# Optimization experiments

Hardware: AMD Instinct MI355X
Metric: run time of the kernel (lower is better)

Reference implementation:

```python
import jax, jax.numpy as jnp
import numpy as np

T, B, IN, H, OUT = 345, 128, 13, 128, 9

# snnTorch ATan surrogate spike: forward = heaviside(x), backward = 1/(1+(pi*x)^2) (alpha=2)
@jax.custom_vjp
def spike_fn(x):
    return (x > 0).astype(x.dtype)

def _spike_fwd(x):
    return spike_fn(x), x

def _spike_bwd(x, g):
    return (g / (1.0 + (jnp.pi * x) ** 2),)

spike_fn.defvjp(_spike_fwd, _spike_bwd)


def setup_inputs() -> dict:
    key = jax.random.key(0)
    ks = jax.random.split(key, 5)
    x = jax.random.normal(ks[0], (B, IN, T), dtype=jnp.float32)
    # PyTorch Linear init: U(-1/sqrt(fan_in), 1/sqrt(fan_in))
    lim1 = 1.0 / np.sqrt(IN)
    lim2 = 1.0 / np.sqrt(H)
    W1 = jax.random.uniform(ks[1], (H, IN), minval=-lim1, maxval=lim1, dtype=jnp.float32)
    b1 = jax.random.uniform(ks[2], (H,), minval=-lim1, maxval=lim1, dtype=jnp.float32)
    W2 = jax.random.uniform(ks[3], (OUT, H), minval=-lim2, maxval=lim2, dtype=jnp.float32)
    b2 = jax.random.uniform(ks[4], (OUT,), minval=-lim2, maxval=lim2, dtype=jnp.float32)
    beta1 = jnp.float32(0.9)
    thr1 = jnp.float32(1.0)
    beta2 = jnp.float32(0.9)
    thr2 = jnp.float32(1.0)
    return {"x": x, "W1": W1, "b1": b1, "W2": W2, "b2": b2,
            "beta1": beta1, "thr1": thr1, "beta2": beta2, "thr2": thr2}


def reference(x, W1, b1, W2, b2, beta1, thr1, beta2, thr2):
    # Precompute fc1 for all steps: (T, B, H)
    cur1_all = jnp.einsum('bct,hc->tbh', x, W1) + b1
    bt1 = jnp.clip(beta1, 0.0, 1.0)
    bt2 = jnp.clip(beta2, 0.0, 1.0)

    def step(carry, cur1):
        mem1, mem2 = carry
        mem1 = bt1 * mem1 + cur1                 # leaky integrate
        spk1 = spike_fn(mem1 - thr1)             # fire
        mem1 = mem1 - spk1 * thr1                # subtract reset
        cur2 = spk1 @ W2.T + b2                  # (B, OUT)
        mem2 = bt2 * mem2 + cur2
        spk2 = spike_fn(mem2 - thr2)
        mem2 = mem2 - spk2 * thr2
        return (mem1, mem2), (spk2, mem2)

    init = (jnp.zeros((B, H), x.dtype), jnp.zeros((B, OUT), x.dtype))
    _, (spk_rec, mem_rec) = jax.lax.scan(step, init, cur1_all)
    return spk_rec, mem_rec  # each (T, B, OUT)
```

## Files before the change

### kernel.cpp

```cpp
#include <hip/hip_runtime.h>

#define T_STEPS 345
#define B_SZ    128
#define IN_SZ   13
#define H_SZ    128
#define OUT_SZ  9
#define XPITCH  16
#define TPAD    384
#define CPAD    388
#define NBO     (B_SZ * OUT_SZ)

__global__ __launch_bounds__(512, 2)
void snn_fused(const float* __restrict__ x, const float* __restrict__ W1,
               const float* __restrict__ b1, const float* __restrict__ W2,
               const float* __restrict__ b2,
               const float* __restrict__ beta1p, const float* __restrict__ thr1p,
               const float* __restrict__ beta2p, const float* __restrict__ thr2p,
               float* __restrict__ out)
{
    const int b    = blockIdx.x >> 1;
    const int half = blockIdx.x & 1;
    const int tid  = threadIdx.x;

    __shared__ float xst[(T_STEPS + 3) * XPITCH];
    __shared__ unsigned long long msh[TPAD * 2];
    __shared__ float c2s[OUT_SZ * CPAD];

    const float* xb = x + (size_t)b * (IN_SZ * T_STEPS);
    for (int i = tid; i < IN_SZ * T_STEPS; i += 512) {
        const int c = i / T_STEPS;
        const int t = i - c * T_STEPS;
        xst[t * XPITCH + c] = xb[i];
    }
    __syncthreads();

    if (tid < 128) {
        const float bt1 = fminf(fmaxf(beta1p[0], 0.0f), 1.0f);
        const float th1 = thr1p[0];

        float w1r[IN_SZ];
#pragma unroll
        for (int c = 0; c < IN_SZ; ++c) w1r[c] = W1[tid * IN_SZ + c];
        const float b1r = b1[tid];

        float mem1 = 0.0f;
        unsigned long long* mp = msh + (tid >> 6);
        const bool store_lane = (tid & 63) == 0;

        const float4* xq = (const float4*)xst;
        float4 a0 = xq[0], a1 = xq[1], a2 = xq[2]; float a3 = xst[12];
        float4 c0 = xq[4], c1 = xq[5], c2 = xq[6]; float c3 = xst[XPITCH + 12];

        int t = 0;
        for (; t < T_STEPS - 1; t += 2) {
            const float xa[IN_SZ] = { a0.x,a0.y,a0.z,a0.w, a1.x,a1.y,a1.z,a1.w,
                                      a2.x,a2.y,a2.z,a2.w, a3 };
            const float xc[IN_SZ] = { c0.x,c0.y,c0.z,c0.w, c1.x,c1.y,c1.z,c1.w,
                                      c2.x,c2.y,c2.z,c2.w, c3 };
            a0 = xq[(t+2)*4+0]; a1 = xq[(t+2)*4+1]; a2 = xq[(t+2)*4+2]; a3 = xst[(t+2)*XPITCH+12];
            c0 = xq[(t+3)*4+0]; c1 = xq[(t+3)*4+1]; c2 = xq[(t+3)*4+2]; c3 = xst[(t+3)*XPITCH+12];

            float cura = b1r, curb = b1r;
#pragma unroll
            for (int c = 0; c < IN_SZ; ++c) {
                cura = fmaf(xa[c], w1r[c], cura);
                curb = fmaf(xc[c], w1r[c], curb);
            }

            mem1 = fmaf(bt1, mem1, cura);
            const bool pa = mem1 > th1;
            const unsigned long long ma = __ballot(pa);
            mem1 = fmaf(pa ? -1.0f : 0.0f, th1, mem1);
            if (store_lane) mp[0] = ma;

            mem1 = fmaf(bt1, mem1, curb);
            const bool pb = mem1 > th1;
            const unsigned long long mb = __ballot(pb);
            mem1 = fmaf(pb ? -1.0f : 0.0f, th1, mem1);
            if (store_lane) mp[2] = mb;

            mp += 4;
        }
        {
            const float xa[IN_SZ] = { a0.x,a0.y,a0.z,a0.w, a1.x,a1.y,a1.z,a1.w,
                                      a2.x,a2.y,a2.z,a2.w, a3 };
            float cura = b1r;
#pragma unroll
            for (int c = 0; c < IN_SZ; ++c) cura = fmaf(xa[c], w1r[c], cura);
            mem1 = fmaf(bt1, mem1, cura);
            const bool pa = mem1 > th1;
            const unsigned long long ma = __ballot(pa);
            if (store_lane) mp[0] = ma;
        }
    }
    __syncthreads();

    {
        const int wave = tid >> 6;
        const int lane = tid & 63;
        const int tstart = half ? 30 : 0;
        const int tend   = half ? 54 : 30;
        for (int task = tstart + wave; task < tend; task += 8) {
            const int o  = task / 6;
            const int w  = task - o * 6;
            const int t  = w * 64 + lane;
            const int tc = (t < T_STEPS) ? t : (T_STEPS - 1);

            const uint4 mm = *(const uint4*)((const char*)msh + (size_t)tc * 16);

            const float* __restrict__ w2row = W2 + o * H_SZ;
            float acc = 0.0f;
#pragma unroll
            for (int h = 0; h < 32; ++h)
                acc = fmaf((float)((mm.x >> h) & 1u), w2row[h], acc);
#pragma unroll
            for (int h = 0; h < 32; ++h)
                acc = fmaf((float)((mm.y >> h) & 1u), w2row[32 + h], acc);
#pragma unroll
            for (int h = 0; h < 32; ++h)
                acc = fmaf((float)((mm.z >> h) & 1u), w2row[64 + h], acc);
#pragma unroll
            for (int h = 0; h < 32; ++h)
                acc = fmaf((float)((mm.w >> h) & 1u), w2row[96 + h], acc);

            c2s[o * CPAD + t] = acc + b2[o];
        }
    }
    __syncthreads();

    {
        const int nrows = half ? 4 : 5;
        if (tid < nrows) {
            const int o = (half ? 5 : 0) + tid;
            const float bt2 = fminf(fmaxf(beta2p[0], 0.0f), 1.0f);
            const float th2 = thr2p[0];
            const int lid = b * OUT_SZ + o;

            const float4* __restrict__ src = (const float4*)(c2s + o * CPAD);
            float* __restrict__ out_spk = out + lid;
            float* __restrict__ out_mem = out + (size_t)T_STEPS * NBO + lid;

            float mem2 = 0.0f;
            float4 f0 = src[0], f1 = src[1], f2 = src[2], f3 = src[3];

            for (int g = 0; g < 88; g += 4) {
                const float4 u0 = f0, u1 = f1, u2 = f2, u3 = f3;
                f0 = src[g + 4]; f1 = src[g + 5]; f2 = src[g + 6]; f3 = src[g + 7];

                const float4 us[4] = { u0, u1, u2, u3 };
#pragma unroll
                for (int j = 0; j < 4; ++j) {
                    const float vv[4] = { us[j].x, us[j].y, us[j].z, us[j].w };
#pragma unroll
                    for (int k = 0; k < 4; ++k) {
                        const int tt = (g + j) * 4 + k;
                        mem2 = fmaf(bt2, mem2, vv[k]);
                        const float s2 = (mem2 > th2) ? 1.0f : 0.0f;
                        mem2 = fmaf(-s2, th2, mem2);
                        if (tt < T_STEPS) {
                            out_spk[(size_t)tt * NBO] = s2;
                            out_mem[(size_t)tt * NBO] = mem2;
                        }
                    }
                }
            }
        }
    }
}

extern "C" void kernel_launch(void* const* d_in, const int* in_sizes, int n_in,
                              void* d_out, int out_size, void* d_ws, size_t ws_size,
                              hipStream_t stream) {
    const float* x     = (const float*)d_in[0];
    const float* W1    = (const float*)d_in[1];
    const float* b1    = (const float*)d_in[2];
    const float* W2    = (const float*)d_in[3];
    const float* b2    = (const float*)d_in[4];
    const float* beta1 = (const float*)d_in[5];
    const float* thr1  = (const float*)d_in[6];
    const float* beta2 = (const float*)d_in[7];
    const float* thr2  = (const float*)d_in[8];
    float* out = (float*)d_out;
    (void)in_sizes; (void)n_in; (void)out_size; (void)d_ws; (void)ws_size;

    snn_fused<<<dim3(B_SZ * 2), dim3(512), 0, stream>>>(
        x, W1, b1, W2, b2, beta1, thr1, beta2, thr2, out);
}
```

Baseline: 123.9 us.

## Pipeline fc1 precompute and layer-2 scan alongside the serial recurrences

Moves the fc1 matmul off the serial mem1 scan. Waves 2-7 compute cur1 for the next 92-step chunk into a double-buffered shared array while waves 0-1 scan the current chunk. The W2 projection is then split into 64-step slices, and wave 7 runs the layer-2 scan on slice s-1 while the other waves compute slice s. The aim is to shorten the serial critical path. In exchange it uses much more shared memory (about 100 KB for the cur1 buffers), which may lower occupancy, and it adds a block barrier per stage.

```diff
diff --git a/kernel.cpp b/kernel.cpp
--- a/kernel.cpp
+++ b/kernel.cpp
@@ -5,10 +5,76 @@
 #define IN_SZ   13
 #define H_SZ    128
 #define OUT_SZ  9
-#define XPITCH  16
-#define TPAD    384
 #define CPAD    388
 #define NBO     (B_SZ * OUT_SZ)
+#define CHUNK   92
+#define BUFR    100
+
+
+__device__ __forceinline__ void emit_cur1(float* __restrict__ buf,
+                                          const float* __restrict__ xst,
+                                          const float (&w1r)[4][IN_SZ],
+                                          const float (&b1r)[4],
+                                          int T0, int L, int hq, int off, int stride)
+{
+    for (int tl = off; tl < L; tl += stride) {
+        const int t = T0 + tl;
+        const float4* xq = (const float4*)(xst + t * 16);
+        const float4 x0 = xq[0], x1 = xq[1], x2 = xq[2];
+        const float x12 = xst[t * 16 + 12];
+        const float xa[IN_SZ] = { x0.x,x0.y,x0.z,x0.w, x1.x,x1.y,x1.z,x1.w,
+                                  x2.x,x2.y,x2.z,x2.w, x12 };
+        float* brow = buf + tl * H_SZ + hq;
+#pragma unroll
+        for (int k2 = 0; k2 < 4; ++k2) {
+            float cur = b1r[k2];
+#pragma unroll
+            for (int c = 0; c < IN_SZ; ++c) cur = fmaf(xa[c], w1r[k2][c], cur);
+            brow[k2 * 32] = cur;
+        }
+    }
+}
+
+__device__ __forceinline__ void scan1_step(float& mem1, float u, float bt1, float th1,
+                                           unsigned long long* __restrict__ msh,
+                                           int t, bool sl, int half)
+{
+    mem1 = fmaf(bt1, mem1, u);
+    const bool p = mem1 > th1;
+    const unsigned long long m = __ballot(p);
+    const float ms = mem1 - th1;
+    mem1 = p ? ms : mem1;
+    if (sl) msh[t * 2 + half] = m;
+}
+
+__device__ __forceinline__ void scan1_chunk(const float* __restrict__ buf,
+                                            unsigned long long* __restrict__ msh,
+                                            int T0, int L, int h,
+                                            float bt1, float th1, float& mem1)
+{
+    const float* cb = buf + h;
+    const bool sl = (h & 63) == 0;
+    const int half = h >> 6;
+    float a0 = cb[0*128], a1 = cb[1*128], a2 = cb[2*128], a3 = cb[3*128];
+    float b0 = cb[4*128], b1v = cb[5*128], b2v = cb[6*128], b3 = cb[7*128];
+    const int fullg = L >> 2;
+    const int rem   = L & 3;
+    for (int g = 0; g < fullg; ++g) {
+        const float u0 = a0, u1 = a1, u2 = a2, u3 = a3;
+        a0 = b0; a1 = b1v; a2 = b2v; a3 = b3;
+        const float* nb = cb + (g + 2) * 4 * 128;
+        b0 = nb[0]; b1v = nb[128]; b2v = nb[256]; b3 = nb[384];
+        const int tb = T0 + g * 4;
+        scan1_step(mem1, u0, bt1, th1, msh, tb + 0, sl, half);
+        scan1_step(mem1, u1, bt1, th1, msh, tb + 1, sl, half);
+        scan1_step(mem1, u2, bt1, th1, msh, tb + 2, sl, half);
+        scan1_step(mem1, u3, bt1, th1, msh, tb + 3, sl, half);
+    }
+    const int tb = T0 + fullg * 4;
+    if (rem > 0) scan1_step(mem1, a0, bt1, th1, msh, tb + 0, sl, half);
+    if (rem > 1) scan1_step(mem1, a1, bt1, th1, msh, tb + 1, sl, half);
+    if (rem > 2) scan1_step(mem1, a2, bt1, th1, msh, tb + 2, sl, half);
+}
 
 __global__ __launch_bounds__(512, 2)
 void snn_fused(const float* __restrict__ x, const float* __restrict__ W1,
@@ -21,147 +87,131 @@
     const int b    = blockIdx.x >> 1;
     const int half = blockIdx.x & 1;
     const int tid  = threadIdx.x;
-
-    __shared__ float xst[(T_STEPS + 3) * XPITCH];
-    __shared__ unsigned long long msh[TPAD * 2];
-    __shared__ float c2s[OUT_SZ * CPAD];
+    const int wid  = tid >> 6;
+    const int lane = tid & 63;
+
+    __shared__ __align__(16) float xst[T_STEPS * 16];
+    __shared__ __align__(16) float cur1s[2][BUFR * H_SZ];
+    __shared__ __align__(16) unsigned long long msh[352 * 2];
+    __shared__ __align__(16) float c2s[OUT_SZ * CPAD];
 
     const float* xb = x + (size_t)b * (IN_SZ * T_STEPS);
     for (int i = tid; i < IN_SZ * T_STEPS; i += 512) {
         const int c = i / T_STEPS;
         const int t = i - c * T_STEPS;
-        xst[t * XPITCH + c] = xb[i];
+        xst[t * 16 + c] = xb[i];
+    }
+    float* W1t = c2s;
+    for (int i = tid; i < IN_SZ * H_SZ; i += 512) {
+        const int h = i / IN_SZ;
+        const int c = i - IN_SZ * h;
+        W1t[c * H_SZ + h] = W1[i];
     }
     __syncthreads();
 
-    if (tid < 128) {
-        const float bt1 = fminf(fmaxf(beta1p[0], 0.0f), 1.0f);
-        const float th1 = thr1p[0];
-
-        float w1r[IN_SZ];
-#pragma unroll
-        for (int c = 0; c < IN_SZ; ++c) w1r[c] = W1[tid * IN_SZ + c];
-        const float b1r = b1[tid];
-
-        float mem1 = 0.0f;
-        unsigned long long* mp = msh + (tid >> 6);
-        const bool store_lane = (tid & 63) == 0;
-
-        const float4* xq = (const float4*)xst;
-        float4 a0 = xq[0], a1 = xq[1], a2 = xq[2]; float a3 = xst[12];
-        float4 c0 = xq[4], c1 = xq[5], c2 = xq[6]; float c3 = xst[XPITCH + 12];
-
-        int t = 0;
-        for (; t < T_STEPS - 1; t += 2) {
-            const float xa[IN_SZ] = { a0.x,a0.y,a0.z,a0.w, a1.x,a1.y,a1.z,a1.w,
-                                      a2.x,a2.y,a2.z,a2.w, a3 };
-            const float xc[IN_SZ] = { c0.x,c0.y,c0.z,c0.w, c1.x,c1.y,c1.z,c1.w,
-                                      c2.x,c2.y,c2.z,c2.w, c3 };
-            a0 = xq[(t+2)*4+0]; a1 = xq[(t+2)*4+1]; a2 = xq[(t+2)*4+2]; a3 = xst[(t+2)*XPITCH+12];
-            c0 = xq[(t+3)*4+0]; c1 = xq[(t+3)*4+1]; c2 = xq[(t+3)*4+2]; c3 = xst[(t+3)*XPITCH+12];
-
-            float cura = b1r, curb = b1r;
-#pragma unroll
-            for (int c = 0; c < IN_SZ; ++c) {
-                cura = fmaf(xa[c], w1r[c], cura);
-                curb = fmaf(xc[c], w1r[c], curb);
+    const int hq = tid & 31;
+    float w1r[4][IN_SZ];
+    float b1r[4];
+#pragma unroll
+    for (int k2 = 0; k2 < 4; ++k2) {
+        b1r[k2] = b1[hq + 32 * k2];
+#pragma unroll
+        for (int c = 0; c < IN_SZ; ++c) w1r[k2][c] = W1t[c * H_SZ + hq + 32 * k2];
+    }
+    const float bt1 = fminf(fmaxf(beta1p[0], 0.0f), 1.0f);
+    const float th1 = thr1p[0];
+
+    emit_cur1(cur1s[0], xst, w1r, b1r, 0, CHUNK, hq, tid >> 5, 16);
+    __syncthreads();
+
+    float mem1 = 0.0f;
+    for (int k = 0; k < 4; ++k) {
+        if (tid < 128) {
+            const int L = (k < 3) ? CHUNK : (T_STEPS - 3 * CHUNK);
+            scan1_chunk(cur1s[k & 1], msh, k * CHUNK, L, tid, bt1, th1, mem1);
+        } else if (k < 3) {
+            const int kn = k + 1;
+            const int L = (kn < 3) ? CHUNK : (T_STEPS - 3 * CHUNK);
+            emit_cur1(cur1s[kn & 1], xst, w1r, b1r, kn * CHUNK, L, hq, (tid >> 5) - 4, 12);
+        }
+        __syncthreads();
+    }
+
+    const int obase  = half ? 5 : 0;
+    const int ntasks = half ? 4 : 5;
+    const float bt2 = fminf(fmaxf(beta2p[0], 0.0f), 1.0f);
+    const float th2 = thr2p[0];
+
+    float mem2 = 0.0f;
+    const int o_sc = obase + lane;
+    float* out_spk = out + (size_t)b * OUT_SZ + o_sc;
+    float* out_mem = out_spk + (size_t)T_STEPS * NBO;
+    const float4* src4 = (const float4*)(c2s + lane * CPAD);
+
+    for (int s = 0; s < 6; ++s) {
+        if (wid < 7) {
+            if (wid < ntasks) {
+                const int o = obase + wid;
+                const int t = s * 64 + lane;
+                const int tc = (t < T_STEPS) ? t : (T_STEPS - 1);
+                const uint4 mm = *(const uint4*)((const char*)msh + (size_t)tc * 16);
+                const float* __restrict__ w2row = W2 + o * H_SZ;
+                float acc = 0.0f;
+#pragma unroll
+                for (int h = 0; h < 32; ++h)
+                    acc = fmaf((float)((mm.x >> h) & 1u), w2row[h], acc);
+#pragma unroll
+                for (int h = 0; h < 32; ++h)
+                    acc = fmaf((float)((mm.y >> h) & 1u), w2row[32 + h], acc);
+#pragma unroll
+                for (int h = 0; h < 32; ++h)
+                    acc = fmaf((float)((mm.z >> h) & 1u), w2row[64 + h], acc);
+#pragma unroll
+                for (int h = 0; h < 32; ++h)
+                    acc = fmaf((float)((mm.w >> h) & 1u), w2row[96 + h], acc);
+                c2s[wid * CPAD + t] = acc + b2[o];
             }
-
-            mem1 = fmaf(bt1, mem1, cura);
-            const bool pa = mem1 > th1;
-            const unsigned long long ma = __ballot(pa);
-            mem1 = fmaf(pa ? -1.0f : 0.0f, th1, mem1);
-            if (store_lane) mp[0] = ma;
-
-            mem1 = fmaf(bt1, mem1, curb);
-            const bool pb = mem1 > th1;
-            const unsigned long long mb = __ballot(pb);
-            mem1 = fmaf(pb ? -1.0f : 0.0f, th1, mem1);
-            if (store_lane) mp[2] = mb;
-
-            mp += 4;
-        }
-        {
-            const float xa[IN_SZ] = { a0.x,a0.y,a0.z,a0.w, a1.x,a1.y,a1.z,a1.w,
-                                      a2.x,a2.y,a2.z,a2.w, a3 };
-            float cura = b1r;
-#pragma unroll
-            for (int c = 0; c < IN_SZ; ++c) cura = fmaf(xa[c], w1r[c], cura);
-            mem1 = fmaf(bt1, mem1, cura);
-            const bool pa = mem1 > th1;
-            const unsigned long long ma = __ballot(pa);
-            if (store_lane) mp[0] = ma;
-        }
-    }
-    __syncthreads();
-
-    {
-        const int wave = tid >> 6;
-        const int lane = tid & 63;
-        const int tstart = half ? 30 : 0;
-        const int tend   = half ? 54 : 30;
-        for (int task = tstart + wave; task < tend; task += 8) {
-            const int o  = task / 6;
-            const int w  = task - o * 6;
-            const int t  = w * 64 + lane;
-            const int tc = (t < T_STEPS) ? t : (T_STEPS - 1);
-
-            const uint4 mm = *(const uint4*)((const char*)msh + (size_t)tc * 16);
-
-            const float* __restrict__ w2row = W2 + o * H_SZ;
-            float acc = 0.0f;
-#pragma unroll
-            for (int h = 0; h < 32; ++h)
-                acc = fmaf((float)((mm.x >> h) & 1u), w2row[h], acc);
-#pragma unroll
-            for (int h = 0; h < 32; ++h)
-                acc = fmaf((float)((mm.y >> h) & 1u), w2row[32 + h], acc);
-#pragma unroll
-            for (int h = 0; h < 32; ++h)
-                acc = fmaf((float)((mm.z >> h) & 1u), w2row[64 + h], acc);
-#pragma unroll
-            for (int h = 0; h < 32; ++h)
-                acc = fmaf((float)((mm.w >> h) & 1u), w2row[96 + h], acc);
-
-            c2s[o * CPAD + t] = acc + b2[o];
-        }
-    }
-    __syncthreads();
-
-    {
-        const int nrows = half ? 4 : 5;
-        if (tid < nrows) {
-            const int o = (half ? 5 : 0) + tid;
-            const float bt2 = fminf(fmaxf(beta2p[0], 0.0f), 1.0f);
-            const float th2 = thr2p[0];
-            const int lid = b * OUT_SZ + o;
-
-            const float4* __restrict__ src = (const float4*)(c2s + o * CPAD);
-            float* __restrict__ out_spk = out + lid;
-            float* __restrict__ out_mem = out + (size_t)T_STEPS * NBO + lid;
-
-            float mem2 = 0.0f;
-            float4 f0 = src[0], f1 = src[1], f2 = src[2], f3 = src[3];
-
-            for (int g = 0; g < 88; g += 4) {
-                const float4 u0 = f0, u1 = f1, u2 = f2, u3 = f3;
-                f0 = src[g + 4]; f1 = src[g + 5]; f2 = src[g + 6]; f3 = src[g + 7];
-
-                const float4 us[4] = { u0, u1, u2, u3 };
-#pragma unroll
-                for (int j = 0; j < 4; ++j) {
-                    const float vv[4] = { us[j].x, us[j].y, us[j].z, us[j].w };
-#pragma unroll
-                    for (int k = 0; k < 4; ++k) {
-                        const int tt = (g + j) * 4 + k;
-                        mem2 = fmaf(bt2, mem2, vv[k]);
-                        const float s2 = (mem2 > th2) ? 1.0f : 0.0f;
-                        mem2 = fmaf(-s2, th2, mem2);
-                        if (tt < T_STEPS) {
-                            out_spk[(size_t)tt * NBO] = s2;
-                            out_mem[(size_t)tt * NBO] = mem2;
-                        }
-                    }
+        } else if (s > 0 && lane < ntasks) {
+            const int sb = (s - 1) * 16;
+            float4 fA = src4[sb], fB = src4[sb + 1];
+#pragma unroll
+            for (int i = 0; i < 16; ++i) {
+                const float4 u = fA; fA = fB; fB = src4[sb + i + 2];
+                const float vv[4] = { u.x, u.y, u.z, u.w };
+#pragma unroll
+                for (int kk = 0; kk < 4; ++kk) {
+                    const int tt = (s - 1) * 64 + i * 4 + kk;
+                    mem2 = fmaf(bt2, mem2, vv[kk]);
+                    const bool p = mem2 > th2;
+                    const float s2 = p ? 1.0f : 0.0f;
+                    const float ms = mem2 - th2;
+                    mem2 = p ? ms : mem2;
+                    out_spk[(size_t)tt * NBO] = s2;
+                    out_mem[(size_t)tt * NBO] = mem2;
+                }
+            }
+        }
+        __syncthreads();
+    }
+
+    if (wid == 7 && lane < ntasks) {
+        const int sb = 5 * 16;
+        float4 fA = src4[sb], fB = src4[sb + 1];
+#pragma unroll
+        for (int i = 0; i < 16; ++i) {
+            const float4 u = fA; fA = fB; fB = src4[sb + i + 2];
+            const float vv[4] = { u.x, u.y, u.z, u.w };
+#pragma unroll
+            for (int kk = 0; kk < 4; ++kk) {
+                const int tt = 5 * 64 + i * 4 + kk;
+                if (tt < T_STEPS) {
+                    mem2 = fmaf(bt2, mem2, vv[kk]);
+                    const bool p = mem2 > th2;
+                    const float s2 = p ? 1.0f : 0.0f;
+                    const float ms = mem2 - th2;
+                    mem2 = p ? ms : mem2;
+                    out_spk[(size_t)tt * NBO] = s2;
+                    out_mem[(size_t)tt * NBO] = mem2;
                 }
             }
         }
```

Result: faster. 103.7 us (-16.2%).
